# Kernel optimization log

Hardware: AMD Instinct MI355X
Metric: run time of the kernel (lower is better)

## Reference

```python
import jax, jax.numpy as jnp
import numpy as np

N, C = 20000, 512          # num_nodes, in_channels
E_RAND = 140000            # random edges (plus N self loops appended)
B, D = 128, 2              # num_bundles, bundle_dim
T = C // (B * D)           # feature cols per bundle (=2)
GNN_DIM = 512
NBP = B * (D * (D - 1) // 2)  # num_bun_params = 128 (1 angle per bundle since D=2)
MAX_DEG = 4
TAU = 1.0
EPS = 1e-5                 # BatchNorm1d eps


def setup_inputs() -> dict:
    key = jax.random.key(0)
    ks = jax.random.split(key, 8)
    x = jax.random.normal(ks[0], (N, C), jnp.float32)
    # edges: random + self-loops so every node has positive out-degree (finite deg_inv)
    src = jax.random.randint(ks[1], (E_RAND,), 0, N)
    dst = jax.random.randint(ks[2], (E_RAND,), 0, N)
    loop = jnp.arange(N)
    edge_index = jnp.stack([jnp.concatenate([src, loop]),
                            jnp.concatenate([dst, loop])]).astype(jnp.int64)
    s = 0.02
    W1 = jax.random.normal(ks[3], (C, GNN_DIM), jnp.float32) * s   # struct_enc lin1
    b1 = jnp.zeros((GNN_DIM,), jnp.float32)
    W2 = jax.random.normal(ks[4], (GNN_DIM, NBP), jnp.float32) * s # struct_enc lin2
    b2 = jnp.zeros((NBP,), jnp.float32)
    Wlin = jax.random.normal(ks[5], (C, C), jnp.float32) * s       # BuNNConv.lin
    blin = jnp.zeros((C,), jnp.float32)
    gamma = jnp.ones((C,), jnp.float32)                            # BatchNorm weight
    beta = jnp.zeros((C,), jnp.float32)                            # BatchNorm bias
    return dict(x=x, W1=W1, b1=b1, W2=W2, b2=b2, Wlin=Wlin, blin=blin,
                gamma=gamma, beta=beta, edge_index=edge_index)


def reference(x, W1, b1, W2, b2, Wlin, blin, gamma, beta, edge_index):
    src, dst = edge_index[0], edge_index[1]
    # degree of edge_index[0]; edge_weight = deg_inv[row] with row = edge_index[1]
    deg = jax.ops.segment_sum(jnp.ones_like(src, jnp.float32), src, num_segments=N)
    ew = (1.0 / deg)[dst]                                   # [E]

    # struct encoder (num_gnn == 0 branch): Linear -> GELU -> Linear -> 1 angle/bundle
    theta = jax.nn.gelu(x @ W1 + b1, approximate=False) @ W2 + b2   # [N, B]
    c, s = jnp.cos(theta), jnp.sin(theta)
    R = jnp.stack([jnp.stack([c, -s], -1),
                   jnp.stack([s, c], -1)], -2)              # [N, B, 2, 2] orthogonal

    # map into bundle frame
    vf = x.reshape(N, B, D, T)
    vf = jnp.einsum('nbij,nbjt->nbit', R, vf)
    h = vf.reshape(N, C)

    # truncated heat-kernel diffusion via scatter message passing
    cur = h
    for k in range(1, MAX_DEG + 1):
        agg = jax.ops.segment_sum(ew[:, None] * cur[src], dst, num_segments=N)
        cur = (-TAU / k) * (cur - agg)
        h = h + cur

    h = h @ Wlin + blin

    # map back with R^T
    vf = h.reshape(N, B, D, T)
    vf = jnp.einsum('nbji,nbjt->nbit', R, vf)
    h = vf.reshape(N, C)

    h = x + h                                # residual (dropout p = 0.0)
    mean = h.mean(axis=0)                    # BatchNorm1d, training mode, biased var
    var = h.var(axis=0)
    return (h - mean) / jnp.sqrt(var + EPS) * gamma + beta
```

## Files before the change

kernel.cpp:

```cpp
#include <hip/hip_runtime.h>

#define CC   512
#define BB_  128
#define BM 64
#define BN 128

typedef __attribute__((ext_vector_type(8))) short short8;
typedef __attribute__((ext_vector_type(8))) unsigned short u16x8;
typedef __attribute__((ext_vector_type(4))) float f32x4;
typedef __attribute__((ext_vector_type(2))) float f32x2;
typedef __attribute__((ext_vector_type(4))) unsigned short u16x4;

__device__ __forceinline__ unsigned short f2bf(float f) {
  union { float f; unsigned u; } v; v.f = f;
  return (unsigned short)((v.u + 0x7FFFu + ((v.u >> 16) & 1u)) >> 16);
}
__device__ __forceinline__ float bf2f(unsigned short b) {
  union { unsigned u; float f; } v; v.u = ((unsigned)b) << 16;
  return v.f;
}

__device__ __forceinline__ size_t pidx(int row, int k, int K32) {
  return ((size_t)((row >> 4) * K32 + (k >> 5)) << 9) +
         (size_t)(((row & 15) + ((k >> 3) & 3) * 16) << 3) + (k & 7);
}

__global__ void k_zero(int* __restrict__ a, int* __restrict__ b, int* __restrict__ c,
                       float* __restrict__ d, float* __restrict__ e, int n) {
  int i = blockIdx.x * blockDim.x + threadIdx.x;
  if (i < n) { a[i] = 0; b[i] = 0; c[i] = 0; }
  if (i < CC) { d[i] = 0.f; e[i] = 0.f; }
}

__global__ void k_count(const int* __restrict__ src, const int* __restrict__ dst,
                        int* __restrict__ cnt_src, int* __restrict__ cnt_dst, int E) {
  int e = blockIdx.x * blockDim.x + threadIdx.x;
  if (e < E) {
    atomicAdd(&cnt_src[src[e]], 1);
    atomicAdd(&cnt_dst[dst[e]], 1);
  }
}

__global__ __launch_bounds__(1024) void k_scan(const int* __restrict__ cnt,
                                               int* __restrict__ rp, int n) {
  __shared__ int sm[1024];
  int tid = threadIdx.x;
  int chunk = (n + 1023) >> 10;
  int beg = tid * chunk;
  int end = beg + chunk; if (end > n) end = n;
  int s = 0;
  for (int i = beg; i < end && i < n; ++i) s += cnt[i];
  sm[tid] = s;
  __syncthreads();
  for (int off = 1; off < 1024; off <<= 1) {
    int v = (tid >= off) ? sm[tid - off] : 0;
    __syncthreads();
    sm[tid] += v;
    __syncthreads();
  }
  int run = (tid == 0) ? 0 : sm[tid - 1];
  for (int i = beg; i < end && i < n; ++i) { rp[i] = run; run += cnt[i]; }
  if (tid == 0) rp[n] = sm[1023];
}

__global__ void k_fill(const int* __restrict__ src, const int* __restrict__ dst,
                       const int* __restrict__ rp, int* __restrict__ fil,
                       int* __restrict__ col, int E) {
  int e = blockIdx.x * blockDim.x + threadIdx.x;
  if (e < E) {
    int d = dst[e];
    int p = atomicAdd(&fil[d], 1);
    col[rp[d] + p] = src[e];
  }
}

__global__ void k_conv_pan(const float* __restrict__ in, unsigned short* __restrict__ out,
                           int validRows, int total8) {
  int i = blockIdx.x * blockDim.x + threadIdx.x;
  if (i >= total8) return;
  int row = i >> 6;
  int c = (i & 63) << 3;
  u16x8 o;
  if (row < validRows) {
    f32x4 v0 = ((const f32x4*)in)[(i << 1)];
    f32x4 v1 = ((const f32x4*)in)[(i << 1) + 1];
    o[0] = f2bf(v0[0]); o[1] = f2bf(v0[1]); o[2] = f2bf(v0[2]); o[3] = f2bf(v0[3]);
    o[4] = f2bf(v1[0]); o[5] = f2bf(v1[1]); o[6] = f2bf(v1[2]); o[7] = f2bf(v1[3]);
  } else {
    #pragma unroll
    for (int j = 0; j < 8; ++j) o[j] = 0;
  }
  *(u16x8*)&out[pidx(row, c, CC >> 5)] = o;
}

__global__ void k_transconv_all(const float* __restrict__ W1, const float* __restrict__ W2,
                                const float* __restrict__ Wlin,
                                unsigned short* __restrict__ W1t, unsigned short* __restrict__ W2t,
                                unsigned short* __restrict__ Wlt) {
  const float* W; unsigned short* Wt; int Nw;
  if (blockIdx.z == 0)      { W = W1;   Wt = W1t; Nw = 512; }
  else if (blockIdx.z == 1) { W = W2;   Wt = W2t; Nw = 128; if (blockIdx.x >= 4) return; }
  else                      { W = Wlin; Wt = Wlt; Nw = 512; }
  __shared__ float tile[32][33];
  int n0 = blockIdx.x * 32, k0 = blockIdx.y * 32;
  int tx = threadIdx.x, ty = threadIdx.y;
  for (int j = 0; j < 4; ++j)
    tile[ty + j * 8][tx] = W[(k0 + ty + j * 8) * Nw + n0 + tx];
  __syncthreads();
  for (int j = 0; j < 4; ++j)
    Wt[pidx(n0 + ty + j * 8, k0 + tx, 16)] = f2bf(tile[tx][ty + j * 8]);
}

template <int EPI>
__device__ __forceinline__ void epi_store(float v, int row, int colL, void* outp,
                                          const float* x, unsigned short* c0,
                                          int Nw, int nvalid) {
  if (EPI == 0) {
    ((float*)outp)[(size_t)row * Nw + colL] = v;
  } else if (EPI == 1) {
    float g = 0.5f * v * (1.0f + erff(v * 0.70710678118654752f));
    ((unsigned short*)outp)[pidx(row, colL, Nw >> 5)] = f2bf(g);
  } else {
    size_t bidx = (size_t)row * Nw + colL;
    if (row < nvalid) {
      float sv, cv;
      sincosf(v, &sv, &cv);
      f32x2 o; o[0] = cv; o[1] = sv;
      ((f32x2*)outp)[bidx] = o;
      f32x4 xv = ((const f32x4*)x)[bidx];
      u16x4 rr;
      rr[0] = f2bf(cv * xv[0] - sv * xv[2]);
      rr[1] = f2bf(cv * xv[1] - sv * xv[3]);
      rr[2] = f2bf(sv * xv[0] + cv * xv[2]);
      rr[3] = f2bf(sv * xv[1] + cv * xv[3]);
      ((u16x4*)c0)[bidx] = rr;
    } else {
      u16x4 rr; rr[0] = 0; rr[1] = 0; rr[2] = 0; rr[3] = 0;
      ((u16x4*)c0)[bidx] = rr;
    }
  }
}

template <int EPI>
__global__ __launch_bounds__(256) void k_gemm(const unsigned short* __restrict__ A,
                                              const unsigned short* __restrict__ Bt,
                                              const float* __restrict__ bias,
                                              void* __restrict__ outp,
                                              const float* __restrict__ x,
                                              unsigned short* __restrict__ c0,
                                              const f32x2* __restrict__ csr,
                                              float* __restrict__ csum,
                                              float* __restrict__ csq,
                                              int K, int Nw, int nvalid) {
  __shared__ float s_sum[BN], s_sq[BN];
  const int m0 = blockIdx.x * BM;
  const int n0 = blockIdx.y * BN;
  const int tid = threadIdx.x;
  const int wid = tid >> 6, lane = tid & 63;
  const int wr = wid >> 1, wc = wid & 1;
  const int l15 = lane & 15, kg = lane >> 4;
  const int K32 = K >> 5;

  if (EPI == 3) {
    if (tid < BN) { s_sum[tid] = 0.f; s_sq[tid] = 0.f; }
    __syncthreads();
  }

  const unsigned short* pa0 = A + (((size_t)((m0 >> 4) + wr * 2 + 0) * K32) << 9) + lane * 8;
  const unsigned short* pa1 = A + (((size_t)((m0 >> 4) + wr * 2 + 1) * K32) << 9) + lane * 8;
  const unsigned short* pb0 = Bt + (((size_t)((n0 >> 4) + wc * 4 + 0) * K32) << 9) + lane * 8;
  const unsigned short* pb1 = Bt + (((size_t)((n0 >> 4) + wc * 4 + 1) * K32) << 9) + lane * 8;
  const unsigned short* pb2 = Bt + (((size_t)((n0 >> 4) + wc * 4 + 2) * K32) << 9) + lane * 8;
  const unsigned short* pb3 = Bt + (((size_t)((n0 >> 4) + wc * 4 + 3) * K32) << 9) + lane * 8;

  f32x4 acc00 = {}, acc01 = {}, acc02 = {}, acc03 = {};
  f32x4 acc10 = {}, acc11 = {}, acc12 = {}, acc13 = {};

  #pragma unroll 4
  for (int kt = 0; kt < K32; ++kt) {
    const size_t o = (size_t)kt << 9;
    short8 af0 = *(const short8*)(pa0 + o);
    short8 af1 = *(const short8*)(pa1 + o);
    short8 bg0 = *(const short8*)(pb0 + o);
    short8 bg1 = *(const short8*)(pb1 + o);
    short8 bg2 = *(const short8*)(pb2 + o);
    short8 bg3 = *(const short8*)(pb3 + o);
    acc00 = __builtin_amdgcn_mfma_f32_16x16x32_bf16(af0, bg0, acc00, 0, 0, 0);
    acc01 = __builtin_amdgcn_mfma_f32_16x16x32_bf16(af0, bg1, acc01, 0, 0, 0);
    acc02 = __builtin_amdgcn_mfma_f32_16x16x32_bf16(af0, bg2, acc02, 0, 0, 0);
    acc03 = __builtin_amdgcn_mfma_f32_16x16x32_bf16(af0, bg3, acc03, 0, 0, 0);
    acc10 = __builtin_amdgcn_mfma_f32_16x16x32_bf16(af1, bg0, acc10, 0, 0, 0);
    acc11 = __builtin_amdgcn_mfma_f32_16x16x32_bf16(af1, bg1, acc11, 0, 0, 0);
    acc12 = __builtin_amdgcn_mfma_f32_16x16x32_bf16(af1, bg2, acc12, 0, 0, 0);
    acc13 = __builtin_amdgcn_mfma_f32_16x16x32_bf16(af1, bg3, acc13, 0, 0, 0);
  }

  if (EPI != 3) {
#define DO_EPI(ACC, MI, NI)                                                     \
  do {                                                                          \
    const int row_ = m0 + wr * 32 + (MI) * 16 + kg * 4;                         \
    const int col_ = n0 + wc * 64 + (NI) * 16 + l15;                            \
    const float b_ = bias[col_];                                                \
    epi_store<EPI>(ACC[0] + b_, row_ + 0, col_, outp, x, c0, Nw, nvalid);       \
    epi_store<EPI>(ACC[1] + b_, row_ + 1, col_, outp, x, c0, Nw, nvalid);       \
    epi_store<EPI>(ACC[2] + b_, row_ + 2, col_, outp, x, c0, Nw, nvalid);       \
    epi_store<EPI>(ACC[3] + b_, row_ + 3, col_, outp, x, c0, Nw, nvalid);       \
  } while (0)

    DO_EPI(acc00, 0, 0); DO_EPI(acc01, 0, 1); DO_EPI(acc02, 0, 2); DO_EPI(acc03, 0, 3);
    DO_EPI(acc10, 1, 0); DO_EPI(acc11, 1, 1); DO_EPI(acc12, 1, 2); DO_EPI(acc13, 1, 3);
#undef DO_EPI
  } else {
    float pS0 = 0.f, pS1 = 0.f, pS2 = 0.f, pS3 = 0.f;
    float pQ0 = 0.f, pQ1 = 0.f, pQ2 = 0.f, pQ3 = 0.f;
    const int bi = (l15 >> 1) & 1;
#define DO_EPI3(ACC, MI, NI, PS, PQ)                                            \
  do {                                                                          \
    const int row_ = m0 + wr * 32 + (MI) * 16 + kg * 4;                         \
    const int col_ = n0 + wc * 64 + (NI) * 16 + l15;                            \
    const float b_ = bias[col_];                                                \
    _Pragma("unroll")                                                           \
    for (int r = 0; r < 4; ++r) {                                               \
      float v = ACC[r] + b_;                                                    \
      float vp = __shfl_xor(v, 2);           \
      int rr_ = row_ + r;                                                       \
      if (rr_ < nvalid) {                                                       \
        f32x2 a = csr[(size_t)rr_ * BB_ + (col_ >> 2)];                         \
        float ov = bi == 0 ? a[0] * v + a[1] * vp : a[0] * v - a[1] * vp;       \
        ov += x[(size_t)rr_ * CC + col_];                                       \
        ((float*)outp)[(size_t)rr_ * CC + col_] = ov;                           \
        PS += ov; PQ += ov * ov;                                                \
      }                                                                         \
    }                                                                           \
  } while (0)

    DO_EPI3(acc00, 0, 0, pS0, pQ0); DO_EPI3(acc01, 0, 1, pS1, pQ1);
    DO_EPI3(acc02, 0, 2, pS2, pQ2); DO_EPI3(acc03, 0, 3, pS3, pQ3);
    DO_EPI3(acc10, 1, 0, pS0, pQ0); DO_EPI3(acc11, 1, 1, pS1, pQ1);
    DO_EPI3(acc12, 1, 2, pS2, pQ2); DO_EPI3(acc13, 1, 3, pS3, pQ3);
#undef DO_EPI3
    const int cb = wc * 64 + l15;
    atomicAdd(&s_sum[cb +  0], pS0); atomicAdd(&s_sq[cb +  0], pQ0);
    atomicAdd(&s_sum[cb + 16], pS1); atomicAdd(&s_sq[cb + 16], pQ1);
    atomicAdd(&s_sum[cb + 32], pS2); atomicAdd(&s_sq[cb + 32], pQ2);
    atomicAdd(&s_sum[cb + 48], pS3); atomicAdd(&s_sq[cb + 48], pQ3);
    __syncthreads();
    if (tid < BN) {
      atomicAdd(&csum[n0 + tid], s_sum[tid]);
      atomicAdd(&csq[n0 + tid], s_sq[tid]);
    }
  }
}

__global__ __launch_bounds__(256) void k_diffuse(const unsigned short* __restrict__ cur,
                                                 unsigned short* __restrict__ nxt,
                                                 const int* __restrict__ cnt_src,
                                                 const int* __restrict__ rp,
                                                 const int* __restrict__ col,
                                                 float coef, int n) {
  int w = threadIdx.x >> 6, lane = threadIdx.x & 63;
  int v = blockIdx.x * 4 + w;
  if (v >= n) return;
  int beg = rp[v], end = rp[v + 1];
  const u16x8* curv = (const u16x8*)cur;
  float s[8] = {0.f,0.f,0.f,0.f,0.f,0.f,0.f,0.f};
  for (int e = beg; e < end; ++e) {
    int u = col[e];
    u16x8 r = curv[(size_t)u * 64 + lane];
    #pragma unroll
    for (int j = 0; j < 8; ++j) s[j] += bf2f(r[j]);
  }
  float di = 1.0f / (float)cnt_src[v];
  u16x8 cv = curv[(size_t)v * 64 + lane];
  u16x8 o;
  #pragma unroll
  for (int j = 0; j < 8; ++j) o[j] = f2bf((bf2f(cv[j]) - s[j] * di) * coef);
  ((u16x8*)nxt)[(size_t)v * 64 + lane] = o;
}

__global__ __launch_bounds__(256) void k_diffuse_final(const unsigned short* __restrict__ c0,
                                                       const unsigned short* __restrict__ c1,
                                                       const unsigned short* __restrict__ c2,
                                                       const unsigned short* __restrict__ cur,
                                                       unsigned short* __restrict__ hb,
                                                       const int* __restrict__ cnt_src,
                                                       const int* __restrict__ rp,
                                                       const int* __restrict__ col,
                                                       float coef, int n) {
  int w = threadIdx.x >> 6, lane = threadIdx.x & 63;
  int v = blockIdx.x * 4 + w;
  if (v >= n) return;
  int beg = rp[v], end = rp[v + 1];
  const u16x8* curv = (const u16x8*)cur;
  float s[8] = {0.f,0.f,0.f,0.f,0.f,0.f,0.f,0.f};
  for (int e = beg; e < end; ++e) {
    int u = col[e];
    u16x8 r = curv[(size_t)u * 64 + lane];
    #pragma unroll
    for (int j = 0; j < 8; ++j) s[j] += bf2f(r[j]);
  }
  float di = 1.0f / (float)cnt_src[v];
  size_t o = (size_t)v * 64 + lane;
  u16x8 cv = curv[o];
  u16x8 a0 = ((const u16x8*)c0)[o];
  u16x8 a1 = ((const u16x8*)c1)[o];
  u16x8 a2 = ((const u16x8*)c2)[o];
  u16x8 hv;
  #pragma unroll
  for (int j = 0; j < 8; ++j) {
    float c3v = bf2f(cv[j]);
    float c4v = (c3v - s[j] * di) * coef;
    hv[j] = f2bf(bf2f(a0[j]) + bf2f(a1[j]) + bf2f(a2[j]) + c3v + c4v);
  }
  *(u16x8*)&hb[pidx(v, lane << 3, CC >> 5)] = hv;
}

__global__ __launch_bounds__(256) void k_norm(float* __restrict__ out,
                                              const float* __restrict__ colsum,
                                              const float* __restrict__ colsq,
                                              const float* __restrict__ gamma,
                                              const float* __restrict__ beta,
                                              float invn, int n4) {
  __shared__ float ssc[CC], ssh[CC];
  int t = threadIdx.x;
  for (int c = t; c < CC; c += 256) {
    float mean = colsum[c] * invn;
    float var = colsq[c] * invn - mean * mean;
    float sc = gamma[c] * rsqrtf(var + 1e-5f);
    ssc[c] = sc;
    ssh[c] = beta[c] - mean * sc;
  }
  __syncthreads();
  int i = blockIdx.x * blockDim.x + t;
  if (i >= n4) return;
  int c4 = i & (CC / 4 - 1);
  f32x4 v = ((f32x4*)out)[i];
  f32x4 sc = *(const f32x4*)&ssc[c4 * 4];
  f32x4 sh = *(const f32x4*)&ssh[c4 * 4];
  ((f32x4*)out)[i] = v * sc + sh;
}

extern "C" void kernel_launch(void* const* d_in, const int* in_sizes, int n_in,
                              void* d_out, int out_size, void* d_ws, size_t ws_size,
                              hipStream_t stream) {
  (void)n_in; (void)out_size; (void)ws_size;
  const float* x    = (const float*)d_in[0];
  const float* W1   = (const float*)d_in[1];
  const float* b1   = (const float*)d_in[2];
  const float* W2   = (const float*)d_in[3];
  const float* b2   = (const float*)d_in[4];
  const float* Wlin = (const float*)d_in[5];
  const float* blin = (const float*)d_in[6];
  const float* gamma = (const float*)d_in[7];
  const float* beta  = (const float*)d_in[8];
  const int*   ei    = (const int*)d_in[9];

  const int n   = in_sizes[0] / CC;
  const int E   = in_sizes[9] / 2;
  const int GNN = in_sizes[2];
  const int NBP = in_sizes[4];
  const int* src = ei;
  const int* dst = ei + E;
  const int mt64 = (n + BM - 1) / BM;
  const int mpad = 20096;
  const size_t SB = (size_t)mpad * CC;

  char* ws = (char*)d_ws;
  size_t off = 0;
  auto alloc = [&](size_t bytes) -> void* {
    void* p = ws + off;
    off = (off + bytes + 255) & ~(size_t)255;
    return p;
  };
  int*   cnt_src = (int*)alloc((size_t)n * 4);
  int*   cnt_dst = (int*)alloc((size_t)n * 4);
  int*   fil     = (int*)alloc((size_t)n * 4);
  int*   rp      = (int*)alloc((size_t)(n + 1) * 4);
  int*   colx    = (int*)alloc((size_t)E * 4);
  float* colsum  = (float*)alloc(CC * 4);
  float* colsq   = (float*)alloc(CC * 4);
  unsigned short* W1t = (unsigned short*)alloc((size_t)GNN * CC * 2);
  unsigned short* W2t = (unsigned short*)alloc((size_t)NBP * GNN * 2);
  unsigned short* Wlt = (unsigned short*)alloc((size_t)CC * CC * 2);
  f32x2* cs = (f32x2*)alloc((size_t)mpad * BB_ * 8);
  unsigned short* c0 = (unsigned short*)alloc(SB * 2);
  unsigned short* c1 = (unsigned short*)alloc(SB * 2);
  unsigned short* c2 = (unsigned short*)alloc(SB * 2);
  unsigned short* c3 = (unsigned short*)alloc(SB * 2);
  unsigned short* hb = (unsigned short*)alloc(SB * 2);
  unsigned short* xb = (unsigned short*)alloc(SB * 2);
  unsigned short* G  = (unsigned short*)alloc(SB * 2);

  k_zero<<<(n + 255) / 256, 256, 0, stream>>>(cnt_src, cnt_dst, fil, colsum, colsq, n);

  k_count<<<(E + 255) / 256, 256, 0, stream>>>(src, dst, cnt_src, cnt_dst, E);
  k_scan<<<1, 1024, 0, stream>>>(cnt_dst, rp, n);
  k_fill<<<(E + 255) / 256, 256, 0, stream>>>(src, dst, rp, fil, colx, E);

  int total8 = mpad * (CC / 8);
  k_conv_pan<<<(total8 + 255) / 256, 256, 0, stream>>>(x, xb, n, total8);
  k_transconv_all<<<dim3(16, 16, 3), dim3(32, 8), 0, stream>>>(W1, W2, Wlin, W1t, W2t, Wlt);

  k_gemm<1><<<dim3(mt64, GNN / BN), 256, 0, stream>>>(xb, W1t, b1, (void*)G, nullptr, nullptr,
                                                      nullptr, nullptr, nullptr, CC, GNN, n);
  k_gemm<2><<<dim3(mt64, NBP / BN), 256, 0, stream>>>(G, W2t, b2, (void*)cs, x, c0,
                                                      nullptr, nullptr, nullptr, GNN, NBP, n);

  k_diffuse<<<(n + 3) / 4, 256, 0, stream>>>(c0, c1, cnt_src, rp, colx, -1.0f, n);
  k_diffuse<<<(n + 3) / 4, 256, 0, stream>>>(c1, c2, cnt_src, rp, colx, -0.5f, n);
  k_diffuse<<<(n + 3) / 4, 256, 0, stream>>>(c2, c3, cnt_src, rp, colx, -(1.0f / 3.0f), n);
  k_diffuse_final<<<(n + 3) / 4, 256, 0, stream>>>(c0, c1, c2, c3, hb, cnt_src, rp, colx, -0.25f, n);

  k_gemm<3><<<dim3(mt64, CC / BN), 256, 0, stream>>>(hb, Wlt, blin, d_out, x, nullptr,
                                                     cs, colsum, colsq, CC, CC, n);

  int nb = n * BB_;
  k_norm<<<(nb + 255) / 256, 256, 0, stream>>>((float*)d_out, colsum, colsq, gamma, beta,
                                               1.0f / (float)n, nb);
}
```

Measured before the change: 323.9 us.

## Make GEMM persistent with register-resident weight fragments over full K

Rewrites the MFMA GEMM so each block owns a 32-column slice of the weight matrix. The block keeps that slice's bf16 fragments in registers for the entire K=512, then loops persistently over 64-row M tiles, with each wave computing a 16x32 output tile per iteration. This removes repeated weight loads and enables a smaller, fixed-size grid. In exchange it needs very high register pressure and rereads each A tile from global or L2 memory for every column slice, since A reuse drops from four N subtiles to two. K is now hardcoded to 512.

```diff
diff --git a/kernel.cpp b/kernel.cpp
--- a/kernel.cpp
+++ b/kernel.cpp
@@ -2,8 +2,7 @@
 
 #define CC   512
 #define BB_  128
-#define BM 64
-#define BN 128
+#define K32C 16
 
 typedef __attribute__((ext_vector_type(8))) short short8;
 typedef __attribute__((ext_vector_type(8))) unsigned short u16x8;
@@ -141,111 +140,92 @@
   }
 }
 
+#define R16(F) F(0) F(1) F(2) F(3) F(4) F(5) F(6) F(7) F(8) F(9) F(10) F(11) F(12) F(13) F(14) F(15)
+
 template <int EPI>
-__global__ __launch_bounds__(256) void k_gemm(const unsigned short* __restrict__ A,
-                                              const unsigned short* __restrict__ Bt,
-                                              const float* __restrict__ bias,
-                                              void* __restrict__ outp,
-                                              const float* __restrict__ x,
-                                              unsigned short* __restrict__ c0,
-                                              const f32x2* __restrict__ csr,
-                                              float* __restrict__ csum,
-                                              float* __restrict__ csq,
-                                              int K, int Nw, int nvalid) {
-  __shared__ float s_sum[BN], s_sq[BN];
-  const int m0 = blockIdx.x * BM;
-  const int n0 = blockIdx.y * BN;
+__global__ __launch_bounds__(256, 2) void k_gemm(const unsigned short* __restrict__ A,
+                                                 const unsigned short* __restrict__ Bt,
+                                                 const float* __restrict__ bias,
+                                                 void* __restrict__ outp,
+                                                 const float* __restrict__ x,
+                                                 unsigned short* __restrict__ c0,
+                                                 const f32x2* __restrict__ csr,
+                                                 float* __restrict__ csum,
+                                                 float* __restrict__ csq,
+                                                 int MT, int Nw, int nvalid) {
+  __shared__ float s_sum[32], s_sq[32];
+  const int n0 = blockIdx.y * 32;
   const int tid = threadIdx.x;
   const int wid = tid >> 6, lane = tid & 63;
-  const int wr = wid >> 1, wc = wid & 1;
   const int l15 = lane & 15, kg = lane >> 4;
-  const int K32 = K >> 5;
+  const size_t lo = (size_t)lane * 8;
 
   if (EPI == 3) {
-    if (tid < BN) { s_sum[tid] = 0.f; s_sq[tid] = 0.f; }
+    if (tid < 32) { s_sum[tid] = 0.f; s_sq[tid] = 0.f; }
     __syncthreads();
   }
 
-  const unsigned short* pa0 = A + (((size_t)((m0 >> 4) + wr * 2 + 0) * K32) << 9) + lane * 8;
-  const unsigned short* pa1 = A + (((size_t)((m0 >> 4) + wr * 2 + 1) * K32) << 9) + lane * 8;
-  const unsigned short* pb0 = Bt + (((size_t)((n0 >> 4) + wc * 4 + 0) * K32) << 9) + lane * 8;
-  const unsigned short* pb1 = Bt + (((size_t)((n0 >> 4) + wc * 4 + 1) * K32) << 9) + lane * 8;
-  const unsigned short* pb2 = Bt + (((size_t)((n0 >> 4) + wc * 4 + 2) * K32) << 9) + lane * 8;
-  const unsigned short* pb3 = Bt + (((size_t)((n0 >> 4) + wc * 4 + 3) * K32) << 9) + lane * 8;
-
-  f32x4 acc00 = {}, acc01 = {}, acc02 = {}, acc03 = {};
-  f32x4 acc10 = {}, acc11 = {}, acc12 = {}, acc13 = {};
-
-  #pragma unroll 4
-  for (int kt = 0; kt < K32; ++kt) {
-    const size_t o = (size_t)kt << 9;
-    short8 af0 = *(const short8*)(pa0 + o);
-    short8 af1 = *(const short8*)(pa1 + o);
-    short8 bg0 = *(const short8*)(pb0 + o);
-    short8 bg1 = *(const short8*)(pb1 + o);
-    short8 bg2 = *(const short8*)(pb2 + o);
-    short8 bg3 = *(const short8*)(pb3 + o);
-    acc00 = __builtin_amdgcn_mfma_f32_16x16x32_bf16(af0, bg0, acc00, 0, 0, 0);
-    acc01 = __builtin_amdgcn_mfma_f32_16x16x32_bf16(af0, bg1, acc01, 0, 0, 0);
-    acc02 = __builtin_amdgcn_mfma_f32_16x16x32_bf16(af0, bg2, acc02, 0, 0, 0);
-    acc03 = __builtin_amdgcn_mfma_f32_16x16x32_bf16(af0, bg3, acc03, 0, 0, 0);
-    acc10 = __builtin_amdgcn_mfma_f32_16x16x32_bf16(af1, bg0, acc10, 0, 0, 0);
-    acc11 = __builtin_amdgcn_mfma_f32_16x16x32_bf16(af1, bg1, acc11, 0, 0, 0);
-    acc12 = __builtin_amdgcn_mfma_f32_16x16x32_bf16(af1, bg2, acc12, 0, 0, 0);
-    acc13 = __builtin_amdgcn_mfma_f32_16x16x32_bf16(af1, bg3, acc13, 0, 0, 0);
-  }
-
-  if (EPI != 3) {
-#define DO_EPI(ACC, MI, NI)                                                     \
-  do {                                                                          \
-    const int row_ = m0 + wr * 32 + (MI) * 16 + kg * 4;                         \
-    const int col_ = n0 + wc * 64 + (NI) * 16 + l15;                            \
-    const float b_ = bias[col_];                                                \
-    epi_store<EPI>(ACC[0] + b_, row_ + 0, col_, outp, x, c0, Nw, nvalid);       \
-    epi_store<EPI>(ACC[1] + b_, row_ + 1, col_, outp, x, c0, Nw, nvalid);       \
-    epi_store<EPI>(ACC[2] + b_, row_ + 2, col_, outp, x, c0, Nw, nvalid);       \
-    epi_store<EPI>(ACC[3] + b_, row_ + 3, col_, outp, x, c0, Nw, nvalid);       \
-  } while (0)
-
-    DO_EPI(acc00, 0, 0); DO_EPI(acc01, 0, 1); DO_EPI(acc02, 0, 2); DO_EPI(acc03, 0, 3);
-    DO_EPI(acc10, 1, 0); DO_EPI(acc11, 1, 1); DO_EPI(acc12, 1, 2); DO_EPI(acc13, 1, 3);
-#undef DO_EPI
-  } else {
-    float pS0 = 0.f, pS1 = 0.f, pS2 = 0.f, pS3 = 0.f;
-    float pQ0 = 0.f, pQ1 = 0.f, pQ2 = 0.f, pQ3 = 0.f;
-    const int bi = (l15 >> 1) & 1;
-#define DO_EPI3(ACC, MI, NI, PS, PQ)                                            \
-  do {                                                                          \
-    const int row_ = m0 + wr * 32 + (MI) * 16 + kg * 4;                         \
-    const int col_ = n0 + wc * 64 + (NI) * 16 + l15;                            \
-    const float b_ = bias[col_];                                                \
-    _Pragma("unroll")                                                           \
-    for (int r = 0; r < 4; ++r) {                                               \
-      float v = ACC[r] + b_;                                                    \
-      float vp = __shfl_xor(v, 2);           \
-      int rr_ = row_ + r;                                                       \
-      if (rr_ < nvalid) {                                                       \
-        f32x2 a = csr[(size_t)rr_ * BB_ + (col_ >> 2)];                         \
-        float ov = bi == 0 ? a[0] * v + a[1] * vp : a[0] * v - a[1] * vp;       \
-        ov += x[(size_t)rr_ * CC + col_];                                       \
-        ((float*)outp)[(size_t)rr_ * CC + col_] = ov;                           \
-        PS += ov; PQ += ov * ov;                                                \
-      }                                                                         \
-    }                                                                           \
-  } while (0)
-
-    DO_EPI3(acc00, 0, 0, pS0, pQ0); DO_EPI3(acc01, 0, 1, pS1, pQ1);
-    DO_EPI3(acc02, 0, 2, pS2, pQ2); DO_EPI3(acc03, 0, 3, pS3, pQ3);
-    DO_EPI3(acc10, 1, 0, pS0, pQ0); DO_EPI3(acc11, 1, 1, pS1, pQ1);
-    DO_EPI3(acc12, 1, 2, pS2, pQ2); DO_EPI3(acc13, 1, 3, pS3, pQ3);
-#undef DO_EPI3
-    const int cb = wc * 64 + l15;
-    atomicAdd(&s_sum[cb +  0], pS0); atomicAdd(&s_sq[cb +  0], pQ0);
-    atomicAdd(&s_sum[cb + 16], pS1); atomicAdd(&s_sq[cb + 16], pQ1);
-    atomicAdd(&s_sum[cb + 32], pS2); atomicAdd(&s_sq[cb + 32], pQ2);
-    atomicAdd(&s_sum[cb + 48], pS3); atomicAdd(&s_sq[cb + 48], pQ3);
+  const size_t pb0 = (size_t)(n0 >> 4) * K32C;
+  const size_t pb1 = pb0 + K32C;
+#define BL(KT) short8 B0_##KT = *(const short8*)(Bt + ((pb0 + KT) << 9) + lo); \
+               short8 B1_##KT = *(const short8*)(Bt + ((pb1 + KT) << 9) + lo);
+  R16(BL)
+#undef BL
+
+  const int col0 = n0 + l15;
+  const int col1 = n0 + 16 + l15;
+  const float bb0 = bias[col0];
+  const float bb1 = bias[col1];
+  const int bi = (l15 >> 1) & 1;
+  float pS0 = 0.f, pQ0 = 0.f, pS1 = 0.f, pQ1 = 0.f;
+
+  for (int mt = blockIdx.x; mt < MT; mt += gridDim.x) {
+    const size_t pa = (size_t)(mt * 4 + wid) * K32C;
+#define AL(KT) short8 A_##KT = *(const short8*)(A + ((pa + KT) << 9) + lo);
+    R16(AL)
+#undef AL
+    f32x4 acc0 = {}, acc1 = {};
+#define MM(KT) acc0 = __builtin_amdgcn_mfma_f32_16x16x32_bf16(A_##KT, B0_##KT, acc0, 0, 0, 0); \
+               acc1 = __builtin_amdgcn_mfma_f32_16x16x32_bf16(A_##KT, B1_##KT, acc1, 0, 0, 0);
+    R16(MM)
+#undef MM
+
+    const int rowb = mt * 64 + wid * 16 + kg * 4;
+    if (EPI != 3) {
+      #pragma unroll
+      for (int r = 0; r < 4; ++r) {
+        epi_store<EPI>(acc0[r] + bb0, rowb + r, col0, outp, x, c0, Nw, nvalid);
+        epi_store<EPI>(acc1[r] + bb1, rowb + r, col1, outp, x, c0, Nw, nvalid);
+      }
+    } else {
+      #pragma unroll
+      for (int r = 0; r < 4; ++r) {
+        float v0 = acc0[r] + bb0;
+        float v1 = acc1[r] + bb1;
+        float vp0 = __shfl_xor(v0, 2);
+        float vp1 = __shfl_xor(v1, 2);
+        int rr_ = rowb + r;
+        if (rr_ < nvalid) {
+          f32x2 a0 = csr[(size_t)rr_ * BB_ + (col0 >> 2)];
+          f32x2 a1 = csr[(size_t)rr_ * BB_ + (col1 >> 2)];
+          float ov0 = bi == 0 ? a0[0] * v0 + a0[1] * vp0 : a0[0] * v0 - a0[1] * vp0;
+          float ov1 = bi == 0 ? a1[0] * v1 + a1[1] * vp1 : a1[0] * v1 - a1[1] * vp1;
+          ov0 += x[(size_t)rr_ * CC + col0];
+          ov1 += x[(size_t)rr_ * CC + col1];
+          ((float*)outp)[(size_t)rr_ * CC + col0] = ov0;
+          ((float*)outp)[(size_t)rr_ * CC + col1] = ov1;
+          pS0 += ov0; pQ0 += ov0 * ov0;
+          pS1 += ov1; pQ1 += ov1 * ov1;
+        }
+      }
+    }
+  }
+
+  if (EPI == 3) {
+    atomicAdd(&s_sum[l15],      pS0); atomicAdd(&s_sq[l15],      pQ0);
+    atomicAdd(&s_sum[16 + l15], pS1); atomicAdd(&s_sq[16 + l15], pQ1);
     __syncthreads();
-    if (tid < BN) {
+    if (tid < 32) {
       atomicAdd(&csum[n0 + tid], s_sum[tid]);
       atomicAdd(&csq[n0 + tid], s_sq[tid]);
     }
@@ -361,8 +341,8 @@
   const int NBP = in_sizes[4];
   const int* src = ei;
   const int* dst = ei + E;
-  const int mt64 = (n + BM - 1) / BM;
   const int mpad = 20096;
+  const int MT = mpad / 64;
   const size_t SB = (size_t)mpad * CC;
 
   char* ws = (char*)d_ws;
@@ -401,18 +381,18 @@
   k_conv_pan<<<(total8 + 255) / 256, 256, 0, stream>>>(x, xb, n, total8);
   k_transconv_all<<<dim3(16, 16, 3), dim3(32, 8), 0, stream>>>(W1, W2, Wlin, W1t, W2t, Wlt);
 
-  k_gemm<1><<<dim3(mt64, GNN / BN), 256, 0, stream>>>(xb, W1t, b1, (void*)G, nullptr, nullptr,
-                                                      nullptr, nullptr, nullptr, CC, GNN, n);
-  k_gemm<2><<<dim3(mt64, NBP / BN), 256, 0, stream>>>(G, W2t, b2, (void*)cs, x, c0,
-                                                      nullptr, nullptr, nullptr, GNN, NBP, n);
+  k_gemm<1><<<dim3(80, GNN / 32), 256, 0, stream>>>(xb, W1t, b1, (void*)G, nullptr, nullptr,
+                                                    nullptr, nullptr, nullptr, MT, GNN, n);
+  k_gemm<2><<<dim3(157, NBP / 32), 256, 0, stream>>>(G, W2t, b2, (void*)cs, x, c0,
+                                                     nullptr, nullptr, nullptr, MT, NBP, n);
 
   k_diffuse<<<(n + 3) / 4, 256, 0, stream>>>(c0, c1, cnt_src, rp, colx, -1.0f, n);
   k_diffuse<<<(n + 3) / 4, 256, 0, stream>>>(c1, c2, cnt_src, rp, colx, -0.5f, n);
   k_diffuse<<<(n + 3) / 4, 256, 0, stream>>>(c2, c3, cnt_src, rp, colx, -(1.0f / 3.0f), n);
   k_diffuse_final<<<(n + 3) / 4, 256, 0, stream>>>(c0, c1, c2, c3, hb, cnt_src, rp, colx, -0.25f, n);
 
-  k_gemm<3><<<dim3(mt64, CC / BN), 256, 0, stream>>>(hb, Wlt, blin, d_out, x, nullptr,
-                                                     cs, colsum, colsq, CC, CC, n);
+  k_gemm<3><<<dim3(80, CC / 32), 256, 0, stream>>>(hb, Wlt, blin, d_out, x, nullptr,
+                                                   cs, colsum, colsq, MT, CC, n);
 
   int nb = n * BB_;
   k_norm<<<(nb + 255) / 256, 256, 0, stream>>>((float*)d_out, colsum, colsq, gamma, beta,
```

After: 363.5 us. +12.2%, slower.
